# Performance work log

Measured on AMD Instinct MI355X. Metric: run time of the kernel, lower is better.

## Reference

```python
import jax, jax.numpy as jnp
import numpy as np

FRACTION_BITS = 16
INTEGER_BITS = 16
DELTA = 2.0 ** (-(FRACTION_BITS / 2))  # 2^-8
BOUND = 2.0 ** (INTEGER_BITS - 1)      # 2^15


def round_to_fixed(x):
    # floor(x/delta + 0.5), clipped to [-2^15, 2^15-1], rescaled
    rounded = jnp.floor(x / DELTA + 0.5)
    return jnp.clip(rounded, -BOUND, BOUND - 1) * DELTA


def setup_inputs() -> dict:
    key = jax.random.key(0)
    k_x, k_sh, k_sg, k_b = jax.random.split(key, 4)
    N, IN, OUT = 8192, 4096, 4096
    x = jax.random.normal(k_x, (N, IN), dtype=jnp.float32)
    shift = jax.random.uniform(k_sh, (OUT, IN), minval=-10.0, maxval=-1.0, dtype=jnp.float32)
    sign = jax.random.uniform(k_sg, (OUT, IN), minval=-1.0, maxval=0.0, dtype=jnp.float32)
    bound = 1.0 / np.sqrt(IN)
    bias = jax.random.uniform(k_b, (OUT,), minval=-bound, maxval=bound, dtype=jnp.float32)
    return {"x": x, "shift": shift, "sign": sign, "bias": bias}


def reference(x, shift, sign, bias):
    # fixed-point quantization of activations and bias (fallback float path)
    x_q = round_to_fixed(x)
    b_q = round_to_fixed(bias)
    # power-of-two weight: v = 2^round(shift) * (-1)^round(sign)
    v = jnp.exp2(jnp.round(shift)) * jnp.where(jnp.round(sign) % 2 == 0, 1.0, -1.0)
    out = x_q @ v.T + b_q[None, :]
    return out
```

## Files before the change

### kernel.cpp

```cpp
#include <hip/hip_runtime.h>


typedef short short8 __attribute__((ext_vector_type(8)));
typedef unsigned short ushort4v __attribute__((ext_vector_type(4)));
typedef float floatx4 __attribute__((ext_vector_type(4)));

__device__ __forceinline__ float qfix(float x) {
    float r = floorf(x * 256.0f + 0.5f);
    r = fminf(fmaxf(r, -32768.0f), 32767.0f);
    return r * 0.00390625f;
}

__device__ __forceinline__ unsigned short f2bf(float f) {
    unsigned int b = __builtin_bit_cast(unsigned int, f);
    b += 0x7FFFu + ((b >> 16) & 1u);
    return (unsigned short)(b >> 16);
}

__global__ __launch_bounds__(256) void quantize_x_kernel(
        const float* __restrict__ x, unsigned short* __restrict__ xq, int n4) {
    int i = blockIdx.x * 256 + threadIdx.x;
    const int stride = gridDim.x * 256;
    for (; i < n4; i += stride) {
        float4 v = reinterpret_cast<const float4*>(x)[i];
        ushort4v o;
        o[0] = f2bf(qfix(v.x));
        o[1] = f2bf(qfix(v.y));
        o[2] = f2bf(qfix(v.z));
        o[3] = f2bf(qfix(v.w));
        reinterpret_cast<ushort4v*>(xq)[i] = o;
    }
}

__global__ __launch_bounds__(256) void make_v_kernel(
        const float* __restrict__ shift, const float* __restrict__ sign,
        unsigned short* __restrict__ v, int n4) {
    int i = blockIdx.x * 256 + threadIdx.x;
    const int stride = gridDim.x * 256;
    for (; i < n4; i += stride) {
        float4 sh = reinterpret_cast<const float4*>(shift)[i];
        float4 sg = reinterpret_cast<const float4*>(sign)[i];
        ushort4v o;
        o[0] = f2bf(ldexpf((rintf(sg.x) == 0.0f) ? 1.0f : -1.0f, (int)rintf(sh.x)));
        o[1] = f2bf(ldexpf((rintf(sg.y) == 0.0f) ? 1.0f : -1.0f, (int)rintf(sh.y)));
        o[2] = f2bf(ldexpf((rintf(sg.z) == 0.0f) ? 1.0f : -1.0f, (int)rintf(sh.z)));
        o[3] = f2bf(ldexpf((rintf(sg.w) == 0.0f) ? 1.0f : -1.0f, (int)rintf(sh.w)));
        reinterpret_cast<ushort4v*>(v)[i] = o;
    }
}

__device__ __forceinline__ void async_load16(const void* g, void* l) {
    __builtin_amdgcn_global_load_lds(
        (const __attribute__((address_space(1))) unsigned int*)g,
        (__attribute__((address_space(3))) unsigned int*)l,
        16, 0, 0);
}

#define STAGE(P, DST) async_load16((P), (DST) + t * 8)
#define STAGE_TILE(NS)  do {                                              \
    STAGE(pA0, (NS));            STAGE(pB0, (NS) + 8192);                 \
    STAGE(pB1, (NS) + 12288);    STAGE(pA1, (NS) + 4096);                 \
    pA0 += 32; pA1 += 32; pB0 += 32; pB1 += 32; } while (0)

#define FENCE() asm volatile("" ::: "memory")
#define VM8()  do { FENCE(); __builtin_amdgcn_s_waitcnt(0x0F78); FENCE(); } while (0)
#define VM4()  do { FENCE(); __builtin_amdgcn_s_waitcnt(0x0F74); FENCE(); } while (0)
#define VM0()  do { FENCE(); __builtin_amdgcn_s_waitcnt(0x0F70); FENCE(); } while (0)
#define BAR()  do { FENCE(); __builtin_amdgcn_s_barrier(); FENCE(); } while (0)

__global__ __launch_bounds__(512, 2) void gemm8_kernel(
        const unsigned short* __restrict__ A,
        const unsigned short* __restrict__ B,
        const float* __restrict__ bias,
        float* __restrict__ C,
        int M, int N, int K) {
    extern __shared__ unsigned short smem[];
    const int t = threadIdx.x;
    const int lane = t & 63;
    const int w = t >> 6;
    const int wrow = w >> 2;
    const int wcol = w & 3;
    const int fr  = lane & 15;
    const int kb  = lane >> 4;

    const int nwg = gridDim.x;
    const int bid = blockIdx.x;
    const int cpx = nwg >> 3;
    const int swz = (bid & 7) * cpx + (bid >> 3);
    const int ntN = N >> 8;
    const int bm = (swz / ntN) << 8;
    const int bn = (swz % ntN) << 8;

    const int r0  = t >> 2;
    const int cbo = ((t & 3) ^ ((t >> 3) & 3)) * 8;
    const unsigned short* pA0 = A + (size_t)(bm +       r0) * K + cbo;
    const unsigned short* pA1 = A + (size_t)(bm + 128 + r0) * K + cbo;
    const unsigned short* pB0 = B + (size_t)(bn +       r0) * K + cbo;
    const unsigned short* pB1 = B + (size_t)(bn + 128 + r0) * K + cbo;

    const int xk = ((kb ^ ((fr >> 1) & 3)) << 4);
    const char* sbase = (const char*)smem;
    const char* aRow = sbase + (wrow * 64 + fr) * 64 + xk;
    const char* bR0  = sbase + 16384 + (wcol * 32 +      fr) * 64 + xk;
    const char* bR1  = sbase + 16384 + (wcol * 32 + 16 + fr) * 64 + xk;

    STAGE_TILE(smem);
    STAGE_TILE(smem + 16384);
    STAGE_TILE(smem + 32768);
    VM8();

    floatx4 acc[2][2][4][2] = {};
    const int NT = K >> 5;

    for (int T = 0; T < NT; ++T) {
        BAR();
        const int sb = (T & 3) << 15;

        short8 af0[4], af1[4], bf0[2], bf1[2];
        #pragma unroll
        for (int mf = 0; mf < 4; ++mf) {
            af0[mf] = *reinterpret_cast<const short8*>(aRow + sb +        mf * 1024);
            af1[mf] = *reinterpret_cast<const short8*>(aRow + sb + 8192 + mf * 1024);
        }
        bf0[0] = *reinterpret_cast<const short8*>(bR0 + sb);
        bf0[1] = *reinterpret_cast<const short8*>(bR1 + sb);
        bf1[0] = *reinterpret_cast<const short8*>(bR0 + sb + 8192);
        bf1[1] = *reinterpret_cast<const short8*>(bR1 + sb + 8192);

        if (T < NT - 3)
            STAGE_TILE(smem + (((T + 3) & 3) << 14));

        #pragma unroll
        for (int mf = 0; mf < 4; ++mf)
          #pragma unroll
          for (int nf = 0; nf < 2; ++nf) {
            acc[0][0][mf][nf] = __builtin_amdgcn_mfma_f32_16x16x32_bf16(
                af0[mf], bf0[nf], acc[0][0][mf][nf], 0, 0, 0);
            acc[0][1][mf][nf] = __builtin_amdgcn_mfma_f32_16x16x32_bf16(
                af0[mf], bf1[nf], acc[0][1][mf][nf], 0, 0, 0);
            acc[1][1][mf][nf] = __builtin_amdgcn_mfma_f32_16x16x32_bf16(
                af1[mf], bf1[nf], acc[1][1][mf][nf], 0, 0, 0);
            acc[1][0][mf][nf] = __builtin_amdgcn_mfma_f32_16x16x32_bf16(
                af1[mf], bf0[nf], acc[1][0][mf][nf], 0, 0, 0);
          }

        if (T < NT - 3)      { VM8(); }
        else if (T == NT - 3){ VM4(); }
        else if (T == NT - 2){ VM0(); }
    }

    #pragma unroll
    for (int qm = 0; qm < 2; ++qm)
      #pragma unroll
      for (int qn = 0; qn < 2; ++qn)
        #pragma unroll
        for (int nf = 0; nf < 2; ++nf) {
            const int gcol = bn + qn * 128 + wcol * 32 + nf * 16 + (lane & 15);
            const float bq = qfix(bias[gcol]);
            #pragma unroll
            for (int mf = 0; mf < 4; ++mf) {
                const int grow = bm + qm * 128 + wrow * 64 + mf * 16 + ((lane >> 4) << 2);
                float* p = C + (size_t)grow * N + gcol;
                #pragma unroll
                for (int r = 0; r < 4; ++r)
                    p[(size_t)r * N] = acc[qm][qn][mf][nf][r] + bq;
            }
        }
}

extern "C" void kernel_launch(void* const* d_in, const int* in_sizes, int n_in,
                              void* d_out, int out_size, void* d_ws, size_t ws_size,
                              hipStream_t stream) {
    const float* x     = (const float*)d_in[0];
    const float* shift = (const float*)d_in[1];
    const float* sign  = (const float*)d_in[2];
    const float* bias  = (const float*)d_in[3];
    float* out = (float*)d_out;

    const int N = in_sizes[3];
    const int K = in_sizes[1] / N;
    const int M = in_sizes[0] / K;

    unsigned short* xq = (unsigned short*)d_ws;
    unsigned short* v  = xq + (size_t)M * K;

    quantize_x_kernel<<<2048, 256, 0, stream>>>(x, xq, M * K / 4);
    make_v_kernel<<<2048, 256, 0, stream>>>(shift, sign, v, N * K / 4);

    (void)hipFuncSetAttribute(reinterpret_cast<const void*>(gemm8_kernel),
                              hipFuncAttributeMaxDynamicSharedMemorySize, 131072);
    const int nblk = (M / 256) * (N / 256);
    gemm8_kernel<<<nblk, 512, 131072, stream>>>(xq, v, bias, out, M, N, K);
}
```

Baseline: 311.1 us.

## Load B fragments directly to registers, stage only A through LDS

B operand fragments are now read from global memory straight into registers, double-buffered across iterations, and no longer pass through LDS. Only A tiles are staged asynchronously into LDS, with a shallower ring and half the dynamic shared memory. The intent is to cut LDS traffic and footprint, which could allow better occupancy. The trade-off is that each wave now issues uncoalesced-ish global loads of B with no reuse across waves (duplicated reads across wrow), and prefetch distance is shorter.

```diff
diff --git a/kernel.cpp b/kernel.cpp
--- a/kernel.cpp
+++ b/kernel.cpp
@@ -56,15 +56,13 @@
         16, 0, 0);
 }
 
-#define STAGE(P, DST) async_load16((P), (DST) + t * 8)
-#define STAGE_TILE(NS)  do {                                              \
-    STAGE(pA0, (NS));            STAGE(pB0, (NS) + 8192);                 \
-    STAGE(pB1, (NS) + 12288);    STAGE(pA1, (NS) + 4096);                 \
-    pA0 += 32; pA1 += 32; pB0 += 32; pB1 += 32; } while (0)
+#define STAGE_A(NS)  do {                                                 \
+    async_load16(pA0, (NS) + t * 8);                                      \
+    async_load16(pA1, (NS) + 4096 + t * 8);                               \
+    pA0 += 32; pA1 += 32; } while (0)
 
 #define FENCE() asm volatile("" ::: "memory")
-#define VM8()  do { FENCE(); __builtin_amdgcn_s_waitcnt(0x0F78); FENCE(); } while (0)
-#define VM4()  do { FENCE(); __builtin_amdgcn_s_waitcnt(0x0F74); FENCE(); } while (0)
+#define VM2()  do { FENCE(); __builtin_amdgcn_s_waitcnt(0x0F72); FENCE(); } while (0)
 #define VM0()  do { FENCE(); __builtin_amdgcn_s_waitcnt(0x0F70); FENCE(); } while (0)
 #define BAR()  do { FENCE(); __builtin_amdgcn_s_barrier(); FENCE(); } while (0)
 
@@ -95,58 +93,73 @@
     const int cbo = ((t & 3) ^ ((t >> 3) & 3)) * 8;
     const unsigned short* pA0 = A + (size_t)(bm +       r0) * K + cbo;
     const unsigned short* pA1 = A + (size_t)(bm + 128 + r0) * K + cbo;
-    const unsigned short* pB0 = B + (size_t)(bn +       r0) * K + cbo;
-    const unsigned short* pB1 = B + (size_t)(bn + 128 + r0) * K + cbo;
+
+    const unsigned short* pB00 = B + (size_t)(bn +       wcol * 32 +      fr) * K + kb * 8;
+    const unsigned short* pB01 = B + (size_t)(bn +       wcol * 32 + 16 + fr) * K + kb * 8;
+    const unsigned short* pB10 = B + (size_t)(bn + 128 + wcol * 32 +      fr) * K + kb * 8;
+    const unsigned short* pB11 = B + (size_t)(bn + 128 + wcol * 32 + 16 + fr) * K + kb * 8;
 
     const int xk = ((kb ^ ((fr >> 1) & 3)) << 4);
     const char* sbase = (const char*)smem;
     const char* aRow = sbase + (wrow * 64 + fr) * 64 + xk;
-    const char* bR0  = sbase + 16384 + (wcol * 32 +      fr) * 64 + xk;
-    const char* bR1  = sbase + 16384 + (wcol * 32 + 16 + fr) * 64 + xk;
-
-    STAGE_TILE(smem);
-    STAGE_TILE(smem + 16384);
-    STAGE_TILE(smem + 32768);
-    VM8();
+
+    STAGE_A(smem);
+    STAGE_A(smem + 8192);
+    short8 bfA[2][2], bfB[2][2];
+    bfA[0][0] = *reinterpret_cast<const short8*>(pB00);
+    bfA[0][1] = *reinterpret_cast<const short8*>(pB01);
+    bfA[1][0] = *reinterpret_cast<const short8*>(pB10);
+    bfA[1][1] = *reinterpret_cast<const short8*>(pB11);
+    pB00 += 32; pB01 += 32; pB10 += 32; pB11 += 32;
+    VM0();
+    BAR();
 
     floatx4 acc[2][2][4][2] = {};
     const int NT = K >> 5;
 
-    for (int T = 0; T < NT; ++T) {
+    auto body = [&](int T, short8 (&bfU)[2][2], short8 (&bfL)[2][2])
+            __attribute__((always_inline)) {
         BAR();
-        const int sb = (T & 3) << 15;
-
-        short8 af0[4], af1[4], bf0[2], bf1[2];
+        const int sb = (T & 3) << 14;
+
+        short8 af0[4], af1[4];
         #pragma unroll
         for (int mf = 0; mf < 4; ++mf) {
             af0[mf] = *reinterpret_cast<const short8*>(aRow + sb +        mf * 1024);
             af1[mf] = *reinterpret_cast<const short8*>(aRow + sb + 8192 + mf * 1024);
         }
-        bf0[0] = *reinterpret_cast<const short8*>(bR0 + sb);
-        bf0[1] = *reinterpret_cast<const short8*>(bR1 + sb);
-        bf1[0] = *reinterpret_cast<const short8*>(bR0 + sb + 8192);
-        bf1[1] = *reinterpret_cast<const short8*>(bR1 + sb + 8192);
-
-        if (T < NT - 3)
-            STAGE_TILE(smem + (((T + 3) & 3) << 14));
+
+        if (T + 1 < NT) {
+            bfL[0][0] = *reinterpret_cast<const short8*>(pB00);
+            bfL[0][1] = *reinterpret_cast<const short8*>(pB01);
+            bfL[1][0] = *reinterpret_cast<const short8*>(pB10);
+            bfL[1][1] = *reinterpret_cast<const short8*>(pB11);
+            pB00 += 32; pB01 += 32; pB10 += 32; pB11 += 32;
+        }
+        if (T + 2 < NT)
+            STAGE_A(smem + ((T + 2) & 3) * 8192);
 
         #pragma unroll
         for (int mf = 0; mf < 4; ++mf)
           #pragma unroll
           for (int nf = 0; nf < 2; ++nf) {
             acc[0][0][mf][nf] = __builtin_amdgcn_mfma_f32_16x16x32_bf16(
-                af0[mf], bf0[nf], acc[0][0][mf][nf], 0, 0, 0);
+                af0[mf], bfU[0][nf], acc[0][0][mf][nf], 0, 0, 0);
             acc[0][1][mf][nf] = __builtin_amdgcn_mfma_f32_16x16x32_bf16(
-                af0[mf], bf1[nf], acc[0][1][mf][nf], 0, 0, 0);
+                af0[mf], bfU[1][nf], acc[0][1][mf][nf], 0, 0, 0);
             acc[1][1][mf][nf] = __builtin_amdgcn_mfma_f32_16x16x32_bf16(
-                af1[mf], bf1[nf], acc[1][1][mf][nf], 0, 0, 0);
+                af1[mf], bfU[1][nf], acc[1][1][mf][nf], 0, 0, 0);
             acc[1][0][mf][nf] = __builtin_amdgcn_mfma_f32_16x16x32_bf16(
-                af1[mf], bf0[nf], acc[1][0][mf][nf], 0, 0, 0);
+                af1[mf], bfU[0][nf], acc[1][0][mf][nf], 0, 0, 0);
           }
 
-        if (T < NT - 3)      { VM8(); }
-        else if (T == NT - 3){ VM4(); }
-        else if (T == NT - 2){ VM0(); }
+        if (T + 2 < NT)      { VM2(); }
+        else if (T + 1 < NT) { VM0(); }
+    };
+
+    for (int T = 0; T < NT; T += 2) {
+        body(T,     bfA, bfB);
+        body(T + 1, bfB, bfA);
     }
 
     #pragma unroll
@@ -188,7 +201,7 @@
     make_v_kernel<<<2048, 256, 0, stream>>>(shift, sign, v, N * K / 4);
 
     (void)hipFuncSetAttribute(reinterpret_cast<const void*>(gemm8_kernel),
-                              hipFuncAttributeMaxDynamicSharedMemorySize, 131072);
+                              hipFuncAttributeMaxDynamicSharedMemorySize, 65536);
     const int nblk = (M / 256) * (N / 256);
-    gemm8_kernel<<<nblk, 512, 131072, stream>>>(xq, v, bias, out, M, N, K);
-}
+    gemm8_kernel<<<nblk, 512, 65536, stream>>>(xq, v, bias, out, M, N, K);
+}
```

New measurement: 476.3 us. +53.1%, slower.
